# Kernel optimization log

Hardware: AMD Instinct MI355X
Metric: run time of the kernel (lower is better)

Reference implementation:

```python
import jax, jax.numpy as jnp
import numpy as np

EPS = 0.05
ITERS = 3
NORM_EPS = 1e-12  # torch F.normalize clamp


def setup_inputs() -> dict:
    key = jax.random.key(0)
    k1, k2, k3, k4 = jax.random.split(key, 4)
    x = jax.random.normal(k1, (16, 768, 64, 64), jnp.float32)
    conv_w = jax.random.normal(k2, (256, 768), jnp.float32) * 0.02  # 1x1 conv kernel [out,in]
    conv_b = jax.random.normal(k3, (256,), jnp.float32) * 0.02
    v = jax.random.normal(k4, (32, 256), jnp.float32)  # [num_clusters, token_dim]
    return {"x": x, "conv_w": conv_w, "conv_b": conv_b, "v": v}


def _l2_normalize(a, axis=-1):
    n = jnp.sqrt(jnp.sum(a * a, axis=axis, keepdims=True))
    return a / jnp.maximum(n, NORM_EPS)


def _log_optimal_transport(scores):
    # scores: [b, m, n]; log-domain Sinkhorn with uniform marginals
    b, m, n = scores.shape
    norm = -jnp.log(jnp.float32(m + n))
    Z = scores / EPS
    u = jnp.full((b, m), 0.0, Z.dtype)
    v = jnp.full((b, n), 0.0, Z.dtype)
    for _ in range(ITERS):
        u = norm - jax.scipy.special.logsumexp(Z + v[:, None, :], axis=2)
        v = norm - jax.scipy.special.logsumexp(Z + u[:, :, None], axis=1)
    return jnp.exp(Z + u[:, :, None] + v[:, None, :] - norm)


def reference(x, conv_w, conv_b, v):
    # 1x1 conv projection: [b, C, H, W] -> [b, D, H, W]
    xp = jnp.einsum('bchw,dc->bdhw', x, conv_w) + conv_b[None, :, None, None]
    b, d, H, W = xp.shape
    x_proj = xp.reshape(b, d, H * W).transpose(0, 2, 1)  # [b, hw, d]
    xf = _l2_normalize(x_proj)  # l2_normalize branch
    w = _l2_normalize(v)        # cluster weights normalized (in-place copy in torch)
    scores = jnp.einsum('bnd,md->bnm', xf, w)  # [b, hw, m]
    weights = _log_optimal_transport(scores.transpose(0, 2, 1)).transpose(0, 2, 1)  # [b, hw, m]
    v_tilde = jnp.einsum('bnd,bnm->bmd', xf, weights)  # [b, m, d]
    return (v_tilde, x_proj)
```

## Files before the change

kernel.cpp:

```cpp
#include <hip/hip_runtime.h>
#include <math.h>

#define NORM_C (-8.3255483f)

typedef __attribute__((ext_vector_type(8))) short bf16x8;
typedef __attribute__((ext_vector_type(4))) float f32x4;

union U8 { uint4 q; unsigned u[4]; bf16x8 v; };

__device__ inline unsigned short f2bf_rne(float f) {
    unsigned u = __float_as_uint(f);
    unsigned r = u + 0x7fffu + ((u >> 16) & 1u);
    return (unsigned short)(r >> 16);
}
__device__ inline unsigned pack_bf2(float lo, float hi) {
    unsigned a = __float_as_uint(lo) + 0x8000u;
    unsigned b = __float_as_uint(hi) + 0x8000u;
    return __builtin_amdgcn_perm(b, a, 0x07060302u);
}

__global__ __launch_bounds__(64) void w_prep(const float* __restrict__ W,
                                             const float* __restrict__ v_in,
                                             unsigned short* __restrict__ Wb,
                                             unsigned short* __restrict__ wnb) {
    const int bx = blockIdx.x, tid = threadIdx.x;
    if (bx < 768) {
        int i = (bx * 64 + tid) * 4;
        float4 w = *(const float4*)(W + i);
        unsigned lo = (unsigned)f2bf_rne(w.x) | ((unsigned)f2bf_rne(w.y) << 16);
        unsigned hi = (unsigned)f2bf_rne(w.z) | ((unsigned)f2bf_rne(w.w) << 16);
        *(uint2*)(Wb + i) = make_uint2(lo, hi);
    } else {
        int row = bx - 768;
        float4 v = *(const float4*)(v_in + row * 256 + tid * 4);
        float s = v.x * v.x + v.y * v.y + v.z * v.z + v.w * v.w;
#pragma unroll
        for (int off = 32; off > 0; off >>= 1) s += __shfl_xor(s, off);
        float inv = 1.0f / fmaxf(sqrtf(s), 1e-12f);
        unsigned lo = (unsigned)f2bf_rne(v.x * inv) | ((unsigned)f2bf_rne(v.y * inv) << 16);
        unsigned hi = (unsigned)f2bf_rne(v.z * inv) | ((unsigned)f2bf_rne(v.w * inv) << 16);
        *(uint2*)(wnb + row * 256 + tid * 4) = make_uint2(lo, hi);
    }
}

__global__ __launch_bounds__(256) void conv_mega(const float* __restrict__ x,
                                                 const unsigned short* __restrict__ Wb,
                                                 const float* __restrict__ bias,
                                                 const unsigned short* __restrict__ wnb,
                                                 float* __restrict__ xp,
                                                 float* __restrict__ inv_norm,
                                                 float* __restrict__ Z,
                                                 float2* __restrict__ u1p) {
    __shared__ unsigned As[256 * 20];
    __shared__ unsigned Bs[128 * 17];
    __shared__ float ssq_s[128];
    __shared__ float invs_s[128];
    __shared__ unsigned xfs[128 * 33];
    __shared__ float2 upart_s[4][32];

    const int tid = threadIdx.x;
    const int lane = tid & 63;
    const int wid = tid >> 6;
    const int wn = wid & 1, wd = wid >> 1;
    const int b = blockIdx.y;
    const int n0 = blockIdx.x * 128;
    const int l15 = lane & 15, l4 = lane >> 4;
    const float* xb = x + (size_t)b * 768 * 4096;

    f32x4 acc[8][4];
#pragma unroll
    for (int i = 0; i < 8; ++i)
#pragma unroll
        for (int j = 0; j < 4; ++j) acc[i][j] = (f32x4){0.f, 0.f, 0.f, 0.f};

    for (int k0 = 0; k0 < 768; k0 += 32) {
        __syncthreads();
#pragma unroll
        for (int i = 0; i < 4; ++i) {
            int f = tid + i * 256;
            int dd = f >> 2, c8 = f & 3;
            uint4 w = *(const uint4*)(Wb + (size_t)dd * 768 + k0 + c8 * 8);
            *(uint4*)&As[dd * 20 + c8 * 4] = w;
        }
#pragma unroll
        for (int i = 0; i < 4; ++i) {
            int f = tid + i * 256;
            int n2 = f & 63, ch = f >> 6;
            const float* p = xb + (size_t)(k0 + 2 * ch) * 4096 + n0 + 2 * n2;
            float2 g0 = *(const float2*)p;
            float2 g1 = *(const float2*)(p + 4096);
            Bs[(2 * n2) * 17 + ch] = pack_bf2(g0.x, g1.x);
            Bs[(2 * n2 + 1) * 17 + ch] = pack_bf2(g0.y, g1.y);
        }
        __syncthreads();

        U8 af[8];
#pragma unroll
        for (int dt = 0; dt < 8; ++dt) {
            int row = wd * 128 + dt * 16 + l15;
            af[dt].q = *(uint4*)&As[row * 20 + l4 * 4];
        }
#pragma unroll
        for (int nt = 0; nt < 4; ++nt) {
            int col = wn * 64 + nt * 16 + l15;
            int base = col * 17 + l4 * 4;
            U8 bf;
            bf.u[0] = Bs[base]; bf.u[1] = Bs[base + 1];
            bf.u[2] = Bs[base + 2]; bf.u[3] = Bs[base + 3];
#pragma unroll
            for (int dt = 0; dt < 8; ++dt)
                acc[dt][nt] = __builtin_amdgcn_mfma_f32_16x16x32_bf16(
                    af[dt].v, bf.v, acc[dt][nt], 0, 0, 0);
        }
    }

    float ssq[4] = {0.f, 0.f, 0.f, 0.f};
#pragma unroll
    for (int dt = 0; dt < 8; ++dt) {
        int d = wd * 128 + dt * 16 + l4 * 4;
        float4 bi = *(const float4*)(bias + d);
#pragma unroll
        for (int nt = 0; nt < 4; ++nt) {
            int n = n0 + wn * 64 + nt * 16 + l15;
            f32x4 o = acc[dt][nt];
            o.x += bi.x; o.y += bi.y; o.z += bi.z; o.w += bi.w;
            acc[dt][nt] = o;
            *(f32x4*)(xp + ((size_t)(b * 4096 + n)) * 256 + d) = o;
            ssq[nt] += o.x * o.x + o.y * o.y + o.z * o.z + o.w * o.w;
        }
    }
#pragma unroll
    for (int nt = 0; nt < 4; ++nt) {
        ssq[nt] += __shfl_xor(ssq[nt], 16);
        ssq[nt] += __shfl_xor(ssq[nt], 32);
    }
    if (wd == 0 && l4 == 0) {
#pragma unroll
        for (int nt = 0; nt < 4; ++nt) ssq_s[wn * 64 + nt * 16 + l15] = ssq[nt];
    }
    __syncthreads();
    if (wd == 1 && l4 == 0) {
#pragma unroll
        for (int nt = 0; nt < 4; ++nt) {
            int nl = wn * 64 + nt * 16 + l15;
            float inv = 1.0f / fmaxf(sqrtf(ssq[nt] + ssq_s[nl]), 1e-12f);
            invs_s[nl] = inv;
            inv_norm[b * 4096 + n0 + nl] = inv;
        }
    }

    f32x4 accz[2][2];
#pragma unroll
    for (int i = 0; i < 2; ++i)
#pragma unroll
        for (int j = 0; j < 2; ++j) accz[i][j] = (f32x4){0.f, 0.f, 0.f, 0.f};

    for (int q = 0; q < 4; ++q) {
        __syncthreads();
        if (wd == (q >> 1)) {
#pragma unroll
            for (int dt4 = 0; dt4 < 4; ++dt4) {
                int dt = (q & 1) * 4 + dt4;
#pragma unroll
                for (int nt = 0; nt < 4; ++nt) {
                    int n = wn * 64 + nt * 16 + l15;
                    float inv = invs_s[n];
                    f32x4 a = acc[dt][nt];
                    int base = n * 33 + dt4 * 8 + l4 * 2;
                    xfs[base]     = pack_bf2(a.x * inv, a.y * inv);
                    xfs[base + 1] = pack_bf2(a.z * inv, a.w * inv);
                }
            }
        }
        __syncthreads();
#pragma unroll
        for (int s = 0; s < 2; ++s) {
            U8 wf[2];
#pragma unroll
            for (int mt = 0; mt < 2; ++mt)
                wf[mt].q = *(const uint4*)(wnb + (mt * 16 + l15) * 256 +
                                           q * 64 + s * 32 + l4 * 8);
#pragma unroll
            for (int sti = 0; sti < 2; ++sti) {
                int st = wid + sti * 4;
                int arow = (st * 16 + l15) * 33 + s * 16 + l4 * 4;
                U8 af;
                af.u[0] = xfs[arow]; af.u[1] = xfs[arow + 1];
                af.u[2] = xfs[arow + 2]; af.u[3] = xfs[arow + 3];
#pragma unroll
                for (int mt = 0; mt < 2; ++mt)
                    accz[sti][mt] = __builtin_amdgcn_mfma_f32_16x16x32_bf16(
                        af.v, wf[mt].v, accz[sti][mt], 0, 0, 0);
            }
        }
    }
#pragma unroll
    for (int sti = 0; sti < 2; ++sti)
#pragma unroll
        for (int mt = 0; mt < 2; ++mt) {
            accz[sti][mt].x *= 20.f; accz[sti][mt].y *= 20.f;
            accz[sti][mt].z *= 20.f; accz[sti][mt].w *= 20.f;
            int m = mt * 16 + l15;
            int st = wid + sti * 4;
            *(f32x4*)&Z[((size_t)(b * 32 + m)) * 4096 + n0 + st * 16 + l4 * 4] =
                accz[sti][mt];
        }
#pragma unroll
    for (int mt = 0; mt < 2; ++mt) {
        float v0[8] = {accz[0][mt].x, accz[0][mt].y, accz[0][mt].z, accz[0][mt].w,
                       accz[1][mt].x, accz[1][mt].y, accz[1][mt].z, accz[1][mt].w};
        float mx = v0[0];
#pragma unroll
        for (int i = 1; i < 8; ++i) mx = fmaxf(mx, v0[i]);
        float s = 0.f;
#pragma unroll
        for (int i = 0; i < 8; ++i) s += __expf(v0[i] - mx);
#pragma unroll
        for (int off = 16; off < 64; off <<= 1) {
            float omx = __shfl_xor(mx, off);
            float os = __shfl_xor(s, off);
            float nm = fmaxf(mx, omx);
            s = s * __expf(mx - nm) + os * __expf(omx - nm);
            mx = nm;
        }
        if (lane < 16) upart_s[wid][mt * 16 + lane] = make_float2(mx, s);
    }
    __syncthreads();
    if (wid == 0 && lane < 32) {
        float2 p = upart_s[0][lane];
        float mx = p.x, s = p.y;
#pragma unroll
        for (int w = 1; w < 4; ++w) {
            float2 qq = upart_s[w][lane];
            float nm = fmaxf(mx, qq.x);
            s = s * __expf(mx - nm) + qq.y * __expf(qq.x - nm);
            mx = nm;
        }
        u1p[((size_t)b * 32 + blockIdx.x) * 32 + lane] = make_float2(mx, s);
    }
}

template <int FIRST>
__global__ __launch_bounds__(512) void sink_v(const float* __restrict__ Z,
                                              const float2* __restrict__ u1p,
                                              const float* __restrict__ u_g,
                                              float* __restrict__ v_g) {
    __shared__ float u_s[32];
    const int tid = threadIdx.x;
    const int b = blockIdx.y;
    const int n = blockIdx.x * 512 + tid;
    if (tid < 32) {
        if (FIRST) {
            float2 p = u1p[((size_t)b * 32) * 32 + tid];
            float mx = p.x, s = p.y;
#pragma unroll 4
            for (int t = 1; t < 32; ++t) {
                float2 q = u1p[((size_t)b * 32 + t) * 32 + tid];
                float nm = fmaxf(mx, q.x);
                s = s * __expf(mx - nm) + q.y * __expf(q.x - nm);
                mx = nm;
            }
            u_s[tid] = NORM_C - (mx + __logf(s));
        } else {
            u_s[tid] = u_g[b * 32 + tid];
        }
    }
    __syncthreads();
    float z[32];
#pragma unroll
    for (int m = 0; m < 32; ++m) z[m] = Z[((size_t)(b * 32 + m)) * 4096 + n] + u_s[m];
    float mx = z[0];
#pragma unroll
    for (int m = 1; m < 32; ++m) mx = fmaxf(mx, z[m]);
    float s = 0.f;
#pragma unroll
    for (int m = 0; m < 32; ++m) s += __expf(z[m] - mx);
    v_g[b * 4096 + n] = NORM_C - (mx + __logf(s));
}

__global__ __launch_bounds__(256) void sink_u(const float* __restrict__ Z,
                                              const float* __restrict__ v_g,
                                              float* __restrict__ u_g) {
    __shared__ float wmx[4], wsum[4];
    const int tid = threadIdx.x;
    const int lane = tid & 63, wid = tid >> 6;
    const int b = blockIdx.x >> 5, m = blockIdx.x & 31;
    const float* zr = Z + ((size_t)(b * 32 + m)) * 4096;
    const float* vr = v_g + b * 4096;

    float z[16];
#pragma unroll
    for (int j = 0; j < 16; ++j) {
        int n = tid + j * 256;
        z[j] = zr[n] + vr[n];
    }
    float mx = z[0];
#pragma unroll
    for (int j = 1; j < 16; ++j) mx = fmaxf(mx, z[j]);
    float s = 0.f;
#pragma unroll
    for (int j = 0; j < 16; ++j) s += __expf(z[j] - mx);
#pragma unroll
    for (int off = 1; off < 64; off <<= 1) {
        float omx = __shfl_xor(mx, off);
        float os = __shfl_xor(s, off);
        float nm = fmaxf(mx, omx);
        s = s * __expf(mx - nm) + os * __expf(omx - nm);
        mx = nm;
    }
    if (lane == 0) { wmx[wid] = mx; wsum[wid] = s; }
    __syncthreads();
    if (tid == 0) {
        float gm = wmx[0], gs = wsum[0];
#pragma unroll
        for (int w = 1; w < 4; ++w) {
            float nm = fmaxf(gm, wmx[w]);
            gs = gs * __expf(gm - nm) + wsum[w] * __expf(wmx[w] - nm);
            gm = nm;
        }
        u_g[b * 32 + m] = NORM_C - (gm + __logf(gs));
    }
}

__global__ __launch_bounds__(256) void vtilde_part_k(const float* __restrict__ xp,
                                                     const float* __restrict__ inv_norm,
                                                     const float* __restrict__ Z,
                                                     const float* __restrict__ u_g,
                                                     float* __restrict__ part) {
    __shared__ float u_s[32];
    __shared__ float v3_s[256];
    __shared__ float inv_s[256];
    __shared__ float wt[64 * 36];
    const int tid = threadIdx.x;
    const int cx = blockIdx.x;
    const int chunk = cx >> 1, dh = cx & 1;
    const int b = blockIdx.y;
    const int n0 = chunk * 256;
    if (tid < 32) u_s[tid] = u_g[b * 32 + tid];
    __syncthreads();
    {
        int n = n0 + tid;
        float z[32];
#pragma unroll
        for (int m = 0; m < 32; ++m)
            z[m] = Z[((size_t)(b * 32 + m)) * 4096 + n] + u_s[m];
        float mx = z[0];
#pragma unroll
        for (int m = 1; m < 32; ++m) mx = fmaxf(mx, z[m]);
        float s = 0.f;
#pragma unroll
        for (int m = 0; m < 32; ++m) s += __expf(z[m] - mx);
        v3_s[tid] = NORM_C - (mx + __logf(s));
        inv_s[tid] = inv_norm[b * 4096 + n];
    }
    __syncthreads();

    const int dg = tid & 31, mq = tid >> 5;
    f32x4 acc[4];
#pragma unroll
    for (int j = 0; j < 4; ++j) acc[j] = (f32x4){0.f, 0.f, 0.f, 0.f};
    const float* xpb = xp + ((size_t)(b * 4096 + n0)) * 256 + dh * 128 + dg * 4;

    for (int t = 0; t < 4; ++t) {
#pragma unroll
        for (int i = 0; i < 8; ++i) {
            int e = tid + i * 256;
            int mW = e >> 6, nn = e & 63;
            int nl = t * 64 + nn;
            wt[nn * 36 + mW] =
                __expf(Z[((size_t)(b * 32 + mW)) * 4096 + n0 + nl] + u_s[mW] +
                       v3_s[nl] - NORM_C) * inv_s[nl];
        }
        __syncthreads();
#pragma unroll 4
        for (int nn = 0; nn < 64; ++nn) {
            float4 xv = *(const float4*)(xpb + (size_t)(t * 64 + nn) * 256);
            float4 wv = *(const float4*)&wt[nn * 36 + mq * 4];
            acc[0].x += wv.x * xv.x; acc[0].y += wv.x * xv.y; acc[0].z += wv.x * xv.z; acc[0].w += wv.x * xv.w;
            acc[1].x += wv.y * xv.x; acc[1].y += wv.y * xv.y; acc[1].z += wv.y * xv.z; acc[1].w += wv.y * xv.w;
            acc[2].x += wv.z * xv.x; acc[2].y += wv.z * xv.y; acc[2].z += wv.z * xv.z; acc[2].w += wv.z * xv.w;
            acc[3].x += wv.w * xv.x; acc[3].y += wv.w * xv.y; acc[3].z += wv.w * xv.z; acc[3].w += wv.w * xv.w;
        }
        __syncthreads();
    }
#pragma unroll
    for (int j = 0; j < 4; ++j) {
        int m = mq * 4 + j;
        *(f32x4*)&part[((size_t)(b * 16 + chunk)) * 8192 + m * 256 + dh * 128 + dg * 4] = acc[j];
    }
}

__global__ __launch_bounds__(256) void vtilde_reduce(const float* __restrict__ part,
                                                     float* __restrict__ out_vt) {
    int o = blockIdx.x * 256 + threadIdx.x;
    int b = o >> 13, r = o & 8191;
    float s = 0.f;
#pragma unroll
    for (int c = 0; c < 16; ++c)
        s += part[((size_t)(b * 16 + c)) * 8192 + r];
    out_vt[o] = s;
}

extern "C" void kernel_launch(void* const* d_in, const int* in_sizes, int n_in,
                              void* d_out, int out_size, void* d_ws, size_t ws_size,
                              hipStream_t stream) {
    const float* x      = (const float*)d_in[0];
    const float* conv_w = (const float*)d_in[1];
    const float* conv_b = (const float*)d_in[2];
    const float* v_in   = (const float*)d_in[3];

    float* out_vt = (float*)d_out;
    float* out_xp = (float*)d_out + 131072;

    float* ws = (float*)d_ws;
    float*          inv_norm = ws;
    unsigned short* Wb       = (unsigned short*)(ws + 65536);
    unsigned short* wnb      = (unsigned short*)(ws + 163840);
    float*          Zbuf     = ws + 167936;
    float2*         u1p      = (float2*)(ws + 2265088);
    float*          u_g      = ws + 2297856;
    float*          v_g      = ws + 2298368;
    float*          part     = ws + 2363904;

    w_prep<<<800, 64, 0, stream>>>(conv_w, v_in, Wb, wnb);
    conv_mega<<<dim3(32, 16), 256, 0, stream>>>(x, Wb, conv_b, wnb, out_xp,
                                                inv_norm, Zbuf, u1p);
    sink_v<1><<<dim3(8, 16), 512, 0, stream>>>(Zbuf, u1p, u_g, v_g);
    sink_u<<<512, 256, 0, stream>>>(Zbuf, v_g, u_g);
    sink_v<0><<<dim3(8, 16), 512, 0, stream>>>(Zbuf, u1p, u_g, v_g);
    sink_u<<<512, 256, 0, stream>>>(Zbuf, v_g, u_g);
    vtilde_part_k<<<dim3(32, 16), 256, 0, stream>>>(out_xp, inv_norm, Zbuf, u_g, part);
    vtilde_reduce<<<512, 256, 0, stream>>>(part, out_vt);
}
```

Measured before the change: 375.7 us.

## Double-buffer conv x tiles, read W from global, fuse Sinkhorn u/v steps

The conv GEMM now double-buffers the x tile in LDS and prefetches the next k-slice into registers while MFMAs run. It also drops the LDS staging of the weight tile and reads A fragments directly from global/L2, so each k-step needs only one barrier. The Sinkhorn v-update and u-update are fused into one sink_step kernel that emits partial logsumexp pairs, and the consumer merges them. This cuts four launches to two and removes the separate u/v buffers. vtilde_part_k caches Z in LDS to avoid reading Z from global twice, at the cost of extra shared memory and per-m wave reductions.

```diff
diff --git a/kernel.cpp b/kernel.cpp
--- a/kernel.cpp
+++ b/kernel.cpp
@@ -51,8 +51,7 @@
                                                  float* __restrict__ inv_norm,
                                                  float* __restrict__ Z,
                                                  float2* __restrict__ u1p) {
-    __shared__ unsigned As[256 * 20];
-    __shared__ unsigned Bs[128 * 17];
+    __shared__ unsigned Bs[2][128 * 17];
     __shared__ float ssq_s[128];
     __shared__ float invs_s[128];
     __shared__ unsigned xfs[128 * 33];
@@ -73,45 +72,55 @@
 #pragma unroll
         for (int j = 0; j < 4; ++j) acc[i][j] = (f32x4){0.f, 0.f, 0.f, 0.f};
 
+    const int n2 = tid & 63;
+    const float* xpt = xb + n0 + 2 * n2;
+    float2 ga[4], gb[4];
+
+    auto LOADX = [&](int k0) {
+#pragma unroll
+        for (int i = 0; i < 4; ++i) {
+            const float* p = xpt + (size_t)(k0 + 2 * (wid + 4 * i)) * 4096;
+            ga[i] = *(const float2*)p;
+            gb[i] = *(const float2*)(p + 4096);
+        }
+    };
+    auto STOREB = [&](int buf) {
+#pragma unroll
+        for (int i = 0; i < 4; ++i) {
+            int ch = wid + 4 * i;
+            Bs[buf][(2 * n2) * 17 + ch]     = pack_bf2(ga[i].x, gb[i].x);
+            Bs[buf][(2 * n2 + 1) * 17 + ch] = pack_bf2(ga[i].y, gb[i].y);
+        }
+    };
+
+    LOADX(0);
+    STOREB(0);
+    __syncthreads();
+    int cur = 0;
     for (int k0 = 0; k0 < 768; k0 += 32) {
-        __syncthreads();
-#pragma unroll
-        for (int i = 0; i < 4; ++i) {
-            int f = tid + i * 256;
-            int dd = f >> 2, c8 = f & 3;
-            uint4 w = *(const uint4*)(Wb + (size_t)dd * 768 + k0 + c8 * 8);
-            *(uint4*)&As[dd * 20 + c8 * 4] = w;
-        }
-#pragma unroll
-        for (int i = 0; i < 4; ++i) {
-            int f = tid + i * 256;
-            int n2 = f & 63, ch = f >> 6;
-            const float* p = xb + (size_t)(k0 + 2 * ch) * 4096 + n0 + 2 * n2;
-            float2 g0 = *(const float2*)p;
-            float2 g1 = *(const float2*)(p + 4096);
-            Bs[(2 * n2) * 17 + ch] = pack_bf2(g0.x, g1.x);
-            Bs[(2 * n2 + 1) * 17 + ch] = pack_bf2(g0.y, g1.y);
-        }
-        __syncthreads();
+        if (k0 + 32 < 768) LOADX(k0 + 32);
 
         U8 af[8];
 #pragma unroll
         for (int dt = 0; dt < 8; ++dt) {
             int row = wd * 128 + dt * 16 + l15;
-            af[dt].q = *(uint4*)&As[row * 20 + l4 * 4];
+            af[dt].q = *(const uint4*)(Wb + (size_t)row * 768 + k0 + l4 * 8);
         }
 #pragma unroll
         for (int nt = 0; nt < 4; ++nt) {
             int col = wn * 64 + nt * 16 + l15;
             int base = col * 17 + l4 * 4;
             U8 bf;
-            bf.u[0] = Bs[base]; bf.u[1] = Bs[base + 1];
-            bf.u[2] = Bs[base + 2]; bf.u[3] = Bs[base + 3];
+            bf.u[0] = Bs[cur][base];     bf.u[1] = Bs[cur][base + 1];
+            bf.u[2] = Bs[cur][base + 2]; bf.u[3] = Bs[cur][base + 3];
 #pragma unroll
             for (int dt = 0; dt < 8; ++dt)
                 acc[dt][nt] = __builtin_amdgcn_mfma_f32_16x16x32_bf16(
                     af[dt].v, bf.v, acc[dt][nt], 0, 0, 0);
         }
+        if (k0 + 32 < 768) STOREB(cur ^ 1);
+        __syncthreads();
+        cur ^= 1;
     }
 
     float ssq[4] = {0.f, 0.f, 0.f, 0.f};
@@ -240,116 +249,113 @@
     }
 }
 
-template <int FIRST>
-__global__ __launch_bounds__(512) void sink_v(const float* __restrict__ Z,
-                                              const float2* __restrict__ u1p,
-                                              const float* __restrict__ u_g,
-                                              float* __restrict__ v_g) {
+template <int NIN>
+__global__ __launch_bounds__(256) void sink_step(const float* __restrict__ Z,
+                                                 const float2* __restrict__ up_in,
+                                                 float2* __restrict__ up_out) {
     __shared__ float u_s[32];
-    const int tid = threadIdx.x;
-    const int b = blockIdx.y;
-    const int n = blockIdx.x * 512 + tid;
-    if (tid < 32) {
-        if (FIRST) {
-            float2 p = u1p[((size_t)b * 32) * 32 + tid];
-            float mx = p.x, s = p.y;
-#pragma unroll 4
-            for (int t = 1; t < 32; ++t) {
-                float2 q = u1p[((size_t)b * 32 + t) * 32 + tid];
-                float nm = fmaxf(mx, q.x);
-                s = s * __expf(mx - nm) + q.y * __expf(q.x - nm);
-                mx = nm;
-            }
-            u_s[tid] = NORM_C - (mx + __logf(s));
-        } else {
-            u_s[tid] = u_g[b * 32 + tid];
-        }
-    }
-    __syncthreads();
-    float z[32];
-#pragma unroll
-    for (int m = 0; m < 32; ++m) z[m] = Z[((size_t)(b * 32 + m)) * 4096 + n] + u_s[m];
-    float mx = z[0];
-#pragma unroll
-    for (int m = 1; m < 32; ++m) mx = fmaxf(mx, z[m]);
-    float s = 0.f;
-#pragma unroll
-    for (int m = 0; m < 32; ++m) s += __expf(z[m] - mx);
-    v_g[b * 4096 + n] = NORM_C - (mx + __logf(s));
-}
-
-__global__ __launch_bounds__(256) void sink_u(const float* __restrict__ Z,
-                                              const float* __restrict__ v_g,
-                                              float* __restrict__ u_g) {
-    __shared__ float wmx[4], wsum[4];
+    __shared__ float2 red_s[4][32];
     const int tid = threadIdx.x;
     const int lane = tid & 63, wid = tid >> 6;
-    const int b = blockIdx.x >> 5, m = blockIdx.x & 31;
-    const float* zr = Z + ((size_t)(b * 32 + m)) * 4096;
-    const float* vr = v_g + b * 4096;
-
-    float z[16];
-#pragma unroll
-    for (int j = 0; j < 16; ++j) {
-        int n = tid + j * 256;
-        z[j] = zr[n] + vr[n];
-    }
-    float mx = z[0];
-#pragma unroll
-    for (int j = 1; j < 16; ++j) mx = fmaxf(mx, z[j]);
+    const int b = blockIdx.y;
+    const int chunk = blockIdx.x;
+    const int n = chunk * 256 + tid;
+
+    if (tid < 32) {
+        float2 p = up_in[((size_t)b * NIN) * 32 + tid];
+        float mx = p.x, s = p.y;
+#pragma unroll 4
+        for (int t = 1; t < NIN; ++t) {
+            float2 q = up_in[((size_t)b * NIN + t) * 32 + tid];
+            float nm = fmaxf(mx, q.x);
+            s = s * __expf(mx - nm) + q.y * __expf(q.x - nm);
+            mx = nm;
+        }
+        u_s[tid] = NORM_C - (mx + __logf(s));
+    }
+    __syncthreads();
+
+    float z[32];
+#pragma unroll
+    for (int m = 0; m < 32; ++m) z[m] = Z[((size_t)(b * 32 + m)) * 4096 + n];
+
+    float mx = z[0] + u_s[0];
+#pragma unroll
+    for (int m = 1; m < 32; ++m) mx = fmaxf(mx, z[m] + u_s[m]);
     float s = 0.f;
 #pragma unroll
-    for (int j = 0; j < 16; ++j) s += __expf(z[j] - mx);
-#pragma unroll
-    for (int off = 1; off < 64; off <<= 1) {
-        float omx = __shfl_xor(mx, off);
-        float os = __shfl_xor(s, off);
-        float nm = fmaxf(mx, omx);
-        s = s * __expf(mx - nm) + os * __expf(omx - nm);
-        mx = nm;
-    }
-    if (lane == 0) { wmx[wid] = mx; wsum[wid] = s; }
-    __syncthreads();
-    if (tid == 0) {
-        float gm = wmx[0], gs = wsum[0];
+    for (int m = 0; m < 32; ++m) s += __expf(z[m] + u_s[m] - mx);
+    float vv = NORM_C - (mx + __logf(s));
+
+#pragma unroll
+    for (int m = 0; m < 32; ++m) {
+        float val = z[m] + vv;
+        float vmx = val;
+#pragma unroll
+        for (int off = 1; off < 64; off <<= 1) vmx = fmaxf(vmx, __shfl_xor(vmx, off));
+        float e = __expf(val - vmx);
+#pragma unroll
+        for (int off = 1; off < 64; off <<= 1) e += __shfl_xor(e, off);
+        if (lane == 0) red_s[wid][m] = make_float2(vmx, e);
+    }
+    __syncthreads();
+    if (tid < 32) {
+        float2 p = red_s[0][tid];
+        float gm = p.x, gs = p.y;
 #pragma unroll
         for (int w = 1; w < 4; ++w) {
-            float nm = fmaxf(gm, wmx[w]);
-            gs = gs * __expf(gm - nm) + wsum[w] * __expf(wmx[w] - nm);
+            float2 q = red_s[w][tid];
+            float nm = fmaxf(gm, q.x);
+            gs = gs * __expf(gm - nm) + q.y * __expf(q.x - nm);
             gm = nm;
         }
-        u_g[b * 32 + m] = NORM_C - (gm + __logf(gs));
+        up_out[((size_t)b * 16 + chunk) * 32 + tid] = make_float2(gm, gs);
     }
 }
 
 __global__ __launch_bounds__(256) void vtilde_part_k(const float* __restrict__ xp,
                                                      const float* __restrict__ inv_norm,
                                                      const float* __restrict__ Z,
-                                                     const float* __restrict__ u_g,
+                                                     const float2* __restrict__ u3p,
                                                      float* __restrict__ part) {
     __shared__ float u_s[32];
     __shared__ float v3_s[256];
     __shared__ float inv_s[256];
+    __shared__ float z_s[32 * 257];
     __shared__ float wt[64 * 36];
     const int tid = threadIdx.x;
     const int cx = blockIdx.x;
     const int chunk = cx >> 1, dh = cx & 1;
     const int b = blockIdx.y;
     const int n0 = chunk * 256;
-    if (tid < 32) u_s[tid] = u_g[b * 32 + tid];
+
+    if (tid < 32) {
+        float2 p = u3p[((size_t)b * 16) * 32 + tid];
+        float gm = p.x, gs = p.y;
+#pragma unroll
+        for (int t = 1; t < 16; ++t) {
+            float2 q = u3p[((size_t)b * 16 + t) * 32 + tid];
+            float nm = fmaxf(gm, q.x);
+            gs = gs * __expf(gm - nm) + q.y * __expf(q.x - nm);
+            gm = nm;
+        }
+        u_s[tid] = NORM_C - (gm + __logf(gs));
+    }
     __syncthreads();
     {
         int n = n0 + tid;
-        float z[32];
-#pragma unroll
-        for (int m = 0; m < 32; ++m)
-            z[m] = Z[((size_t)(b * 32 + m)) * 4096 + n] + u_s[m];
-        float mx = z[0];
-#pragma unroll
-        for (int m = 1; m < 32; ++m) mx = fmaxf(mx, z[m]);
+        float zr[32];
+#pragma unroll
+        for (int m = 0; m < 32; ++m) {
+            zr[m] = Z[((size_t)(b * 32 + m)) * 4096 + n];
+            z_s[m * 257 + tid] = zr[m];
+        }
+        float mx = zr[0] + u_s[0];
+#pragma unroll
+        for (int m = 1; m < 32; ++m) mx = fmaxf(mx, zr[m] + u_s[m]);
         float s = 0.f;
 #pragma unroll
-        for (int m = 0; m < 32; ++m) s += __expf(z[m] - mx);
+        for (int m = 0; m < 32; ++m) s += __expf(zr[m] + u_s[m] - mx);
         v3_s[tid] = NORM_C - (mx + __logf(s));
         inv_s[tid] = inv_norm[b * 4096 + n];
     }
@@ -368,8 +374,7 @@
             int mW = e >> 6, nn = e & 63;
             int nl = t * 64 + nn;
             wt[nn * 36 + mW] =
-                __expf(Z[((size_t)(b * 32 + mW)) * 4096 + n0 + nl] + u_s[mW] +
-                       v3_s[nl] - NORM_C) * inv_s[nl];
+                __expf(z_s[mW * 257 + nl] + u_s[mW] + v3_s[nl] - NORM_C) * inv_s[nl];
         }
         __syncthreads();
 #pragma unroll 4
@@ -418,17 +423,15 @@
     unsigned short* wnb      = (unsigned short*)(ws + 163840);
     float*          Zbuf     = ws + 167936;
     float2*         u1p      = (float2*)(ws + 2265088);
-    float*          u_g      = ws + 2297856;
-    float*          v_g      = ws + 2298368;
-    float*          part     = ws + 2363904;
+    float2*         u2p      = (float2*)(ws + 2297856);
+    float2*         u3p      = (float2*)(ws + 2314240);
+    float*          part     = ws + 2330624;
 
     w_prep<<<800, 64, 0, stream>>>(conv_w, v_in, Wb, wnb);
     conv_mega<<<dim3(32, 16), 256, 0, stream>>>(x, Wb, conv_b, wnb, out_xp,
                                                 inv_norm, Zbuf, u1p);
-    sink_v<1><<<dim3(8, 16), 512, 0, stream>>>(Zbuf, u1p, u_g, v_g);
-    sink_u<<<512, 256, 0, stream>>>(Zbuf, v_g, u_g);
-    sink_v<0><<<dim3(8, 16), 512, 0, stream>>>(Zbuf, u1p, u_g, v_g);
-    sink_u<<<512, 256, 0, stream>>>(Zbuf, v_g, u_g);
-    vtilde_part_k<<<dim3(32, 16), 256, 0, stream>>>(out_xp, inv_norm, Zbuf, u_g, part);
+    sink_step<32><<<dim3(16, 16), 256, 0, stream>>>(Zbuf, u1p, u2p);
+    sink_step<16><<<dim3(16, 16), 256, 0, stream>>>(Zbuf, u2p, u3p);
+    vtilde_part_k<<<dim3(32, 16), 256, 0, stream>>>(out_xp, inv_norm, Zbuf, u3p, part);
     vtilde_reduce<<<512, 256, 0, stream>>>(part, out_vt);
 }
```

Result: slower. 414.9 us (+10.4%).
